# Optimization experiments

Measured on AMD Instinct MI355X. Metric: run time of the kernel, lower is better.

Reference implementation:

```python
import jax, jax.numpy as jnp
import numpy as np

B, S, D, F, A, H, O = 8, 2048, 64, 16, 32, 4, 64
HD = A // H  # head dim = 8
TWO_PI = 2.0 * np.pi


def setup_inputs() -> dict:
    key = jax.random.key(0)
    ks = jax.random.split(key, 10)
    sc = lambda k, sh, fan: (jax.random.normal(k, sh, jnp.float32) / np.sqrt(fan)).astype(jnp.float32)
    Din = D + 2 * D * F  # input width to gate/projection MLPs
    return dict(
        x=jax.random.normal(ks[0], (B, S, D), jnp.float32),
        freq_matrix=jnp.tile(jnp.linspace(1.0, 10.0, F, dtype=jnp.float32)[None, :], (D, 1)),
        phase=jax.random.normal(ks[1], (D, F), jnp.float32),
        freq_scale=jnp.ones((D, F), jnp.float32),
        Wq=sc(ks[2], (A, D), D), bq=jnp.zeros((A,), jnp.float32),          # query_proj
        Wk1=sc(ks[3], (A, 1), 1), bk1=jnp.zeros((A,), jnp.float32),        # key_proj (Linear(1, A))
        Wqi=sc(ks[4], (A, A), A), bqi=jnp.zeros((A,), jnp.float32),        # MHA in-proj (q slice)
        Wki=sc(ks[5], (A, A), A), bki=jnp.zeros((A,), jnp.float32),        # MHA in-proj (k slice)
        Wg=sc(ks[6], (O, Din), Din), bg=jnp.zeros((O,), jnp.float32),      # gate linear
        Wp=sc(ks[7], (O, Din), Din), bp=jnp.zeros((O,), jnp.float32),      # projection linear
    )


def reference(x, freq_matrix, phase, freq_scale, Wq, bq, Wk1, bk1, Wqi, bqi, Wki, bki, Wg, bg, Wp, bp):
    # x: [B, S, D]
    t = jnp.linspace(0.0, 1.0, S, dtype=x.dtype)                 # [S]
    f = freq_matrix * freq_scale                                 # [D, F]
    # fourier signal, batched over all input dims at once
    signal = TWO_PI * t[:, None, None] * f[None] + phase[None]   # [S, D, F]
    sin_f, cos_f = jnp.sin(signal), jnp.cos(signal)

    # MHA attention weights (averaged over heads) -- attn_out is discarded by the module
    queries = jnp.einsum('bsd,ad->bsa', x, Wq) + bq              # [B, S, A]
    q = (jnp.einsum('bsa,ea->bse', queries, Wqi) + bqi).reshape(B, S, H, HD)
    keys = f[:, :, None] * Wk1[None, None, :, 0] + bk1           # [D, F, A] via Linear(1, A)
    k = (jnp.einsum('dfa,ea->dfe', keys, Wki) + bki).reshape(D, F, H, HD)
    scores = jnp.einsum('bshe,dfhe->bdhsf', q, k) / np.sqrt(HD)  # [B, D, H, S, F]
    attn = jax.nn.softmax(scores, axis=-1).mean(axis=2)          # [B, D, S, F] (head-avg)
    aw = jnp.transpose(attn, (0, 2, 1, 3))                       # [B, S, D, F]

    # weighted fourier features; per-dim layout is [sin(F), cos(F)] to match torch cat order
    ff = jnp.concatenate([sin_f[None] * aw, cos_f[None] * aw], axis=-1)  # [B, S, D, 2F]
    ff = ff.reshape(B, S, D * 2 * F)

    ci = jnp.concatenate([x, ff], axis=-1)                       # [B, S, D + 2DF]
    gated = jax.nn.sigmoid(jnp.einsum('bsi,oi->bso', ci, Wg) + bg) * \
            jax.nn.silu(jnp.einsum('bsi,oi->bso', ci, Wp) + bp)
    return x + gated
```

## Files before the change

kernel.cpp:

```cpp
#include <hip/hip_runtime.h>
#include <math.h>

#define SS 2048
#define DIN 2112
#define TOK 16
#define NBLK 1024
#define NTHR 256
#define XSTR 68
#define CSTR 132
#define BFRAG_ELEMS (66 * 8 * 64 * 8)
#define LOG2E 1.4426950408889634f
#define INV2PI 0.15915494309189535f

#define OFF_WP 135168
#define OFF_CP 135424
#define OFF_FV 135680
#define OFF_PH 136192
#define OFF_MX 136704

typedef __attribute__((ext_vector_type(4))) float f32x4;
typedef __attribute__((ext_vector_type(8))) _Float16 f16x8;
typedef __attribute__((ext_vector_type(2))) __fp16 fp16v2;

__device__ __forceinline__ unsigned pkh(float a, float b) {
#if __has_builtin(__builtin_amdgcn_cvt_pkrtz)
    union { fp16v2 h; unsigned u; } r;
    r.h = __builtin_amdgcn_cvt_pkrtz(a, b);
    return r.u;
#else
    union { _Float16 h[2]; unsigned u; } r;
    r.h[0] = (_Float16)a; r.h[1] = (_Float16)b;
    return r.u;
#endif
}

#if __has_builtin(__builtin_amdgcn_exp2f)
#define EXP2(x) __builtin_amdgcn_exp2f(x)
#else
#define EXP2(x) exp2f(x)
#endif
#if __has_builtin(__builtin_amdgcn_rcpf)
#define RCP(x) __builtin_amdgcn_rcpf(x)
#else
#define RCP(x) (1.0f / (x))
#endif
#if __has_builtin(__builtin_amdgcn_sinf)
#define SINR(x) __builtin_amdgcn_sinf(x)
#else
#define SINR(x) __sinf(6.283185307179586f * (x))
#endif

__global__ __launch_bounds__(256) void aff_pre(
    const float* __restrict__ Wq, const float* __restrict__ bq,
    const float* __restrict__ Wk1,
    const float* __restrict__ Wqi, const float* __restrict__ bqi,
    const float* __restrict__ Wki,
    const float* __restrict__ Wg, const float* __restrict__ Wp,
    const float* __restrict__ fm, const float* __restrict__ fs,
    const float* __restrict__ phase,
    float* __restrict__ ws)
{
    _Float16* Bf = (_Float16*)ws;
    const int tid = threadIdx.x;
    const int gid = blockIdx.x * 256 + tid;

    {
        int j  = gid & 7;
        int q  = (gid >> 3) & 3;
        int nl = (gid >> 5) & 15;
        int nt = (gid >> 9) & 7;
        int kt = gid >> 12;
        int k = kt * 32 + q * 8 + j;
        int n = nt * 16 + nl;
        float s = (n < 64) ? Wg[(size_t)n * DIN + k] : Wp[(size_t)(n - 64) * DIN + k];
        int dst = ((kt * 8 + nt) * 64 + q * 16 + nl) * 8 + j;
        Bf[dst] = (_Float16)s;
    }

    if (blockIdx.x == 0) {
        float* WP = ws + OFF_WP;
        float* cP = ws + OFF_CP;
        unsigned* fvh = (unsigned*)(ws + OFF_FV);
        unsigned* phh = (unsigned*)(ws + OFF_PH);
        float* mxg = ws + OFF_MX;

        {
            float4 a = ((const float4*)fm)[tid];
            float4 b = ((const float4*)fs)[tid];
            fvh[tid * 2]     = pkh(a.x * b.x, a.y * b.y);
            fvh[tid * 2 + 1] = pkh(a.z * b.z, a.w * b.w);
            float4 p = ((const float4*)phase)[tid];
            phh[tid * 2]     = pkh(p.x * INV2PI, p.y * INV2PI);
            phh[tid * 2 + 1] = pkh(p.z * INV2PI, p.w * INV2PI);
        }
        if (tid < 64) {
            float mx = -1e30f, mn = 1e30f;
            #pragma unroll
            for (int f = 0; f < 16; ++f) {
                float v = (float)(_Float16)(fm[tid * 16 + f] * fs[tid * 16 + f]);
                mx = fmaxf(mx, v); mn = fminf(mn, v);
            }
            mxg[tid * 2] = mx; mxg[tid * 2 + 1] = mn;
        }

        __shared__ float u[32];
        if (tid < 32) {
            float s = 0.f;
            #pragma unroll
            for (int a = 0; a < 32; ++a) s += Wki[tid * 32 + a] * Wk1[a];
            u[tid] = s;
        }
        __syncthreads();
        {
            const int h = tid >> 6;
            const int d = tid & 63;
            float s = 0.f;
            for (int j = 0; j < 8; ++j) {
                int e = h * 8 + j;
                float wc = 0.f;
                #pragma unroll
                for (int a = 0; a < 32; ++a) wc += Wqi[e * 32 + a] * Wq[a * 64 + d];
                s += u[e] * wc;
            }
            WP[h * 64 + d] = s * 0.35355339059327373f * LOG2E;
            if (d == 0) {
                float sc = 0.f;
                for (int j = 0; j < 8; ++j) {
                    int e = h * 8 + j;
                    float bcv = bqi[e];
                    #pragma unroll
                    for (int a = 0; a < 32; ++a) bcv += Wqi[e * 32 + a] * bq[a];
                    sc += u[e] * bcv;
                }
                cP[h] = sc * 0.35355339059327373f * LOG2E;
            }
        }
    }
}

__global__ __launch_bounds__(NTHR, 3) void aff_main(
    const float* __restrict__ x,
    const float* __restrict__ ws_c,
    const float* __restrict__ bg, const float* __restrict__ bp,
    float* __restrict__ out)
{
    __shared__ __align__(16) float xs[TOK * XSTR];
    __shared__ __align__(16) float Cpart[4 * TOK * CSTR];
    __shared__ __align__(16) float Pl[TOK * 4];
    __shared__ __align__(16) _Float16 fvh[1024];
    __shared__ __align__(16) _Float16 phh[1024];
    __shared__ __align__(16) float mxs[128];

    const f16x8* Bv = (const f16x8*)ws_c;
    const float* WP  = ws_c + OFF_WP;
    const float* cP  = ws_c + OFF_CP;
    const float* mxg = ws_c + OFF_MX;

    const int tid  = threadIdx.x;
    const int lane = tid & 63;
    const int w    = tid >> 6;
    const int t0   = blockIdx.x * TOK;
    const int lm   = lane & 15;
    const int lq   = lane >> 4;
    const int fsel = lq & 1;
    const int hp   = lq >> 1;
    const float qoff = hp ? 0.25f : 0.0f;

    {
        uint2 fv2 = ((const uint2*)(ws_c + OFF_FV))[tid];
        uint2 ph2 = ((const uint2*)(ws_c + OFF_PH))[tid];
        ((uint2*)fvh)[tid] = fv2;
        ((uint2*)phh)[tid] = ph2;
    }
    if (tid < 32) ((float4*)mxs)[tid] = ((const float4*)mxg)[tid];
    {
        int t = tid >> 4, j4 = (tid & 15) * 4;
        float4 xv = *(const float4*)(x + (size_t)(t0 + t) * 64 + j4);
        *(float4*)(xs + t * XSTR + j4) = xv;
    }
    __syncthreads();

    if (tid >= 128) {
        int t2 = tid - 128;
        int t = t2 & 15, dh = (t2 >> 4) & 1, h = t2 >> 5;
        float acc = 0.f;
        const float* wp = WP + h * 64 + dh * 32;
        const float* xr = xs + t * XSTR + dh * 32;
        #pragma unroll 8
        for (int d = 0; d < 32; ++d) acc = fmaf(wp[d], xr[d], acc);
        acc += __shfl_xor(acc, 16);
        if (dh == 0) Pl[t * 4 + h] = acc + cP[h];
    }

    f32x4 acc[8] = {};
    f16x8 B0[8], B1[8];
    auto loadB = [&](int kt, f16x8* Bb) {
        const f16x8* p = Bv + (size_t)kt * 512 + lane;
        #pragma unroll
        for (int nt = 0; nt < 8; ++nt) Bb[nt] = p[nt * 64];
    };

    const int dbase = w * 16;

    if (w < 2) {
        loadB(w, B0);
        union { unsigned u[4]; f16x8 v; } ax;
        const float* xr = xs + lm * XSTR + w * 32 + lq * 8;
        ax.u[0] = pkh(xr[0], xr[1]); ax.u[1] = pkh(xr[2], xr[3]);
        ax.u[2] = pkh(xr[4], xr[5]); ax.u[3] = pkh(xr[6], xr[7]);
        loadB(2 + dbase, B1);
        #pragma unroll
        for (int nt = 0; nt < 8; ++nt)
            acc[nt] = __builtin_amdgcn_mfma_f32_16x16x32_f16(ax.v, B0[nt], acc[nt], 0, 0, 0);
    } else {
        loadB(2 + dbase, B1);
    }
    __syncthreads();

    const float P0 = Pl[lm * 4 + hp * 2];
    const float P1 = Pl[lm * 4 + hp * 2 + 1];
    const float w2 = (float)((t0 + lm) & (SS - 1)) * (1.0f / 2047.0f);

    auto build = [&](int d) -> f16x8 {
        union { uint4 q; _Float16 h[8]; } fu, pu;
        fu.q = *(const uint4*)(fvh + d * 16 + fsel * 8);
        pu.q = *(const uint4*)(phh + d * 16 + fsel * 8);
        const float mxv = mxs[d * 2], mnv = mxs[d * 2 + 1];
        float fl[8], prq[8];
        #pragma unroll
        for (int j = 0; j < 8; ++j) { fl[j] = (float)fu.h[j]; prq[j] = (float)pu.h[j] + qoff; }
        const float m0 = fmaxf(mxv * P0, mnv * P0);
        const float m1 = fmaxf(mxv * P1, mnv * P1);
        float e0[8], e1[8], s0 = 0.f, s1 = 0.f;
        #pragma unroll
        for (int j = 0; j < 8; ++j) { e0[j] = EXP2(fmaf(fl[j], P0, -m0)); s0 += e0[j]; }
        #pragma unroll
        for (int j = 0; j < 8; ++j) { e1[j] = EXP2(fmaf(fl[j], P1, -m1)); s1 += e1[j]; }
        const float z0 = s0 + __shfl_xor(s0, 16);
        const float z1 = s1 + __shfl_xor(s1, 16);
        const float i0 = 0.25f * RCP(z0), i1 = 0.25f * RCP(z1);
        union { unsigned u[4]; f16x8 v; } r;
        #pragma unroll
        for (int jp = 0; jp < 4; ++jp) {
            const int j0 = 2 * jp, j1 = 2 * jp + 1;
            float a0 = fmaf(e1[j0], i1, e0[j0] * i0);
            float a1 = fmaf(e1[j1], i1, e0[j1] * i0);
            a0 += __shfl_xor(a0, 32);
            a1 += __shfl_xor(a1, 32);
            const float X0 = fmaf(w2, fl[j0], prq[j0]);
            const float X1 = fmaf(w2, fl[j1], prq[j1]);
            r.u[jp] = pkh(a0 * SINR(X0), a1 * SINR(X1));
        }
        return r.v;
    };

    #pragma unroll
    for (int i = 0; i < 16; ++i) {
        f16x8* cur = (i & 1) ? B0 : B1;
        f16x8* nxt = (i & 1) ? B1 : B0;
        f16x8 a = build(dbase + i);
        if (i < 15) loadB(2 + dbase + i + 1, nxt);
        #pragma unroll
        for (int nt = 0; nt < 8; ++nt)
            acc[nt] = __builtin_amdgcn_mfma_f32_16x16x32_f16(a, cur[nt], acc[nt], 0, 0, 0);
    }

    {
        float* Cw = Cpart + w * TOK * CSTR;
        #pragma unroll
        for (int nt = 0; nt < 8; ++nt)
            #pragma unroll
            for (int r = 0; r < 4; ++r)
                Cw[(lq * 4 + r) * CSTR + nt * 16 + lm] = acc[nt][r];
    }
    __syncthreads();
    {
        int t = tid >> 4, o0 = (tid & 15) * 4;
        float4 g4 = make_float4(0.f, 0.f, 0.f, 0.f), p4 = g4;
        #pragma unroll
        for (int ww = 0; ww < 4; ++ww) {
            const float* Cw = Cpart + ww * TOK * CSTR + t * CSTR;
            float4 g = *(const float4*)(Cw + o0);
            float4 p = *(const float4*)(Cw + 64 + o0);
            g4.x += g.x; g4.y += g.y; g4.z += g.z; g4.w += g.w;
            p4.x += p.x; p4.y += p.y; p4.z += p.z; p4.w += p.w;
        }
        float4 bg4 = *(const float4*)(bg + o0);
        float4 bp4 = *(const float4*)(bp + o0);
        float4 xr = *(float4*)(xs + t * XSTR + o0);
        float4 o;
        { float g = g4.x + bg4.x, p = p4.x + bp4.x;
          o.x = fmaf(p * RCP(1.f + EXP2(-g * LOG2E)), RCP(1.f + EXP2(-p * LOG2E)), xr.x); }
        { float g = g4.y + bg4.y, p = p4.y + bp4.y;
          o.y = fmaf(p * RCP(1.f + EXP2(-g * LOG2E)), RCP(1.f + EXP2(-p * LOG2E)), xr.y); }
        { float g = g4.z + bg4.z, p = p4.z + bp4.z;
          o.z = fmaf(p * RCP(1.f + EXP2(-g * LOG2E)), RCP(1.f + EXP2(-p * LOG2E)), xr.z); }
        { float g = g4.w + bg4.w, p = p4.w + bp4.w;
          o.w = fmaf(p * RCP(1.f + EXP2(-g * LOG2E)), RCP(1.f + EXP2(-p * LOG2E)), xr.w); }
        *(float4*)(out + (size_t)(t0 + t) * 64 + o0) = o;
    }
}

extern "C" void kernel_launch(void* const* d_in, const int* in_sizes, int n_in,
                              void* d_out, int out_size, void* d_ws, size_t ws_size,
                              hipStream_t stream) {
    (void)in_sizes; (void)n_in; (void)out_size; (void)ws_size;
    const float* x    = (const float*)d_in[0];
    const float* fm   = (const float*)d_in[1];
    const float* phs  = (const float*)d_in[2];
    const float* fs   = (const float*)d_in[3];
    const float* Wq   = (const float*)d_in[4];
    const float* bq   = (const float*)d_in[5];
    const float* Wk1  = (const float*)d_in[6];
    const float* Wqi  = (const float*)d_in[8];
    const float* bqi  = (const float*)d_in[9];
    const float* Wki  = (const float*)d_in[10];
    const float* Wg   = (const float*)d_in[12];
    const float* bg   = (const float*)d_in[13];
    const float* Wp   = (const float*)d_in[14];
    const float* bp   = (const float*)d_in[15];
    float* out = (float*)d_out;
    float* ws  = (float*)d_ws;

    aff_pre<<<BFRAG_ELEMS / 256, 256, 0, stream>>>(Wq, bq, Wk1, Wqi, bqi, Wki, Wg, Wp,
                                                   fm, fs, phs, ws);
    aff_main<<<NBLK, NTHR, 0, stream>>>(x, (const float*)ws, bg, bp, out);
}
```

Measured before the change: 122.4 us.

## Single-buffer B fragments and stop unrolling the main K loop to cut registers

```diff
diff --git a/kernel.cpp b/kernel.cpp
--- a/kernel.cpp
+++ b/kernel.cpp
@@ -180,55 +180,53 @@
     }
     __syncthreads();
 
-    if (tid >= 128) {
-        int t2 = tid - 128;
-        int t = t2 & 15, dh = (t2 >> 4) & 1, h = t2 >> 5;
-        float acc = 0.f;
-        const float* wp = WP + h * 64 + dh * 32;
-        const float* xr = xs + t * XSTR + dh * 32;
-        #pragma unroll 8
-        for (int d = 0; d < 32; ++d) acc = fmaf(wp[d], xr[d], acc);
-        acc += __shfl_xor(acc, 16);
-        if (dh == 0) Pl[t * 4 + h] = acc + cP[h];
-    }
-
     f32x4 acc[8] = {};
-    f16x8 B0[8], B1[8];
-    auto loadB = [&](int kt, f16x8* Bb) {
+    f16x8 B[8];
+    auto loadB = [&](int kt) {
         const f16x8* p = Bv + (size_t)kt * 512 + lane;
         #pragma unroll
-        for (int nt = 0; nt < 8; ++nt) Bb[nt] = p[nt * 64];
+        for (int nt = 0; nt < 8; ++nt) B[nt] = p[nt * 64];
     };
 
     const int dbase = w * 16;
 
     if (w < 2) {
-        loadB(w, B0);
+        loadB(w);
         union { unsigned u[4]; f16x8 v; } ax;
         const float* xr = xs + lm * XSTR + w * 32 + lq * 8;
         ax.u[0] = pkh(xr[0], xr[1]); ax.u[1] = pkh(xr[2], xr[3]);
         ax.u[2] = pkh(xr[4], xr[5]); ax.u[3] = pkh(xr[6], xr[7]);
-        loadB(2 + dbase, B1);
         #pragma unroll
         for (int nt = 0; nt < 8; ++nt)
-            acc[nt] = __builtin_amdgcn_mfma_f32_16x16x32_f16(ax.v, B0[nt], acc[nt], 0, 0, 0);
+            acc[nt] = __builtin_amdgcn_mfma_f32_16x16x32_f16(ax.v, B[nt], acc[nt], 0, 0, 0);
     } else {
-        loadB(2 + dbase, B1);
-    }
+        int t2 = tid - 128;
+        int t = t2 & 15, dh = (t2 >> 4) & 1, h = t2 >> 5;
+        float pacc = 0.f;
+        const float* wp = WP + h * 64 + dh * 32;
+        const float* xr = xs + t * XSTR + dh * 32;
+        #pragma unroll 8
+        for (int d = 0; d < 32; ++d) pacc = fmaf(wp[d], xr[d], pacc);
+        pacc += __shfl_xor(pacc, 16);
+        if (dh == 0) Pl[t * 4 + h] = pacc + cP[h];
+    }
+    loadB(2 + dbase);
     __syncthreads();
 
     const float P0 = Pl[lm * 4 + hp * 2];
     const float P1 = Pl[lm * 4 + hp * 2 + 1];
     const float w2 = (float)((t0 + lm) & (SS - 1)) * (1.0f / 2047.0f);
 
-    auto build = [&](int d) -> f16x8 {
+    #pragma unroll 1
+    for (int i = 0; i < 16; ++i) {
+        const int d = dbase + i;
         union { uint4 q; _Float16 h[8]; } fu, pu;
         fu.q = *(const uint4*)(fvh + d * 16 + fsel * 8);
         pu.q = *(const uint4*)(phh + d * 16 + fsel * 8);
         const float mxv = mxs[d * 2], mnv = mxs[d * 2 + 1];
-        float fl[8], prq[8];
-        #pragma unroll
-        for (int j = 0; j < 8; ++j) { fl[j] = (float)fu.h[j]; prq[j] = (float)pu.h[j] + qoff; }
+        float fl[8];
+        #pragma unroll
+        for (int j = 0; j < 8; ++j) fl[j] = (float)fu.h[j];
         const float m0 = fmaxf(mxv * P0, mnv * P0);
         const float m1 = fmaxf(mxv * P1, mnv * P1);
         float e0[8], e1[8], s0 = 0.f, s1 = 0.f;
@@ -247,22 +245,14 @@
             float a1 = fmaf(e1[j1], i1, e0[j1] * i0);
             a0 += __shfl_xor(a0, 32);
             a1 += __shfl_xor(a1, 32);
-            const float X0 = fmaf(w2, fl[j0], prq[j0]);
-            const float X1 = fmaf(w2, fl[j1], prq[j1]);
+            const float X0 = fmaf(w2, fl[j0], (float)pu.h[j0] + qoff);
+            const float X1 = fmaf(w2, fl[j1], (float)pu.h[j1] + qoff);
             r.u[jp] = pkh(a0 * SINR(X0), a1 * SINR(X1));
         }
-        return r.v;
-    };
-
-    #pragma unroll
-    for (int i = 0; i < 16; ++i) {
-        f16x8* cur = (i & 1) ? B0 : B1;
-        f16x8* nxt = (i & 1) ? B1 : B0;
-        f16x8 a = build(dbase + i);
-        if (i < 15) loadB(2 + dbase + i + 1, nxt);
         #pragma unroll
         for (int nt = 0; nt < 8; ++nt)
-            acc[nt] = __builtin_amdgcn_mfma_f32_16x16x32_f16(a, cur[nt], acc[nt], 0, 0, 0);
+            acc[nt] = __builtin_amdgcn_mfma_f32_16x16x32_f16(r.v, B[nt], acc[nt], 0, 0, 0);
+        loadB(2 + dbase + ((i + 1) & 15));
     }
 
     {
```

Result: faster. 119.7 us (-2.2%).
